# Optimization experiments

Measured on AMD Instinct MI355X. Metric: run time of the kernel, lower is better.

Reference implementation:

```python
import jax, jax.numpy as jnp
import numpy as np

N_NODES = 100000
TYPE_COUNTS = [40000, 40000, 20000]
RAW_DIMS = [512, 256, 128]
D = 64          # node_feature_dim
H = 8           # num_attention_heads
M = 2           # num_metapaths
E = 500000      # edges per metapath
SEM = 128       # semantic_attention_dim
NUM_CLS = 8
T = 40000       # num target nodes
SLOPE = 0.01    # leaky relu slope


def setup_inputs() -> dict:
    key = jax.random.key(0)
    ks = jax.random.split(key, 16)
    inp = {}
    inp['target_nodes'] = jax.random.randint(ks[0], (T,), 0, N_NODES)
    inp['metapath_0'] = jax.random.randint(ks[1], (E, 2), 0, N_NODES)
    inp['metapath_1'] = jax.random.randint(ks[2], (E, 2), 0, N_NODES)
    # contiguous blocks per node type (type t occupies a contiguous index range)
    inp['node_type_mapping'] = jnp.concatenate(
        [jnp.full((c,), t, dtype=jnp.int32) for t, c in enumerate(TYPE_COUNTS)])
    for t, (c, r) in enumerate(zip(TYPE_COUNTS, RAW_DIMS)):
        inp[f'node_feat_{t}'] = jax.random.normal(ks[3 + t], (c, r), dtype=jnp.float32)
        xav = float(np.sqrt(2.0) * np.sqrt(2.0 / (D + r)))
        inp[f'W{t}'] = jax.random.normal(ks[6 + t], (D, r), dtype=jnp.float32) * xav
        inp[f'b{t}'] = jnp.zeros((D,), dtype=jnp.float32)
    inp['node_attention'] = jax.random.normal(ks[9], (M, H, 2 * D), dtype=jnp.float32) * 0.05
    inp['Wsem'] = jax.random.normal(ks[10], (SEM, H * D), dtype=jnp.float32) * 0.05
    inp['bsem'] = jnp.zeros((SEM,), dtype=jnp.float32)
    inp['a_sem'] = jax.random.normal(ks[11], (SEM,), dtype=jnp.float32) * 0.05
    inp['Wcls'] = jax.random.normal(ks[12], (NUM_CLS, H * D), dtype=jnp.float32) * 0.05
    inp['bcls'] = jnp.zeros((NUM_CLS,), dtype=jnp.float32)
    return inp


def _metapath_agg(node_features, mp, attn_vec, target_nodes, n_nodes):
    # mp: [E, 2] (col 0 = neighbor/src, col -1 = current/dst); attn_vec: [H, 2D]
    src = mp[:, 0]
    dst = mp[:, -1]
    h_src = node_features[src]                        # [E, D] gather
    h_dst = node_features[dst]                        # [E, D] gather
    e = jnp.concatenate([h_dst, h_src], axis=-1)      # [E, 2D]
    score = e @ attn_vec.T                            # [E, H]
    score = jnp.where(score > 0, score, SLOPE * score)  # LeakyReLU
    # edge softmax over incoming edges of each destination node (per head)
    m = jax.ops.segment_max(score, dst, num_segments=n_nodes)
    ex = jnp.exp(score - m[dst])
    den = jax.ops.segment_sum(ex, dst, num_segments=n_nodes)
    attn = ex / den[dst]                              # [E, H]
    weighted = h_src[:, None, :] * attn[:, :, None]   # [E, H, D]
    agg = jax.ops.segment_sum(weighted, dst, num_segments=n_nodes)  # [N, H, D]
    return agg[target_nodes]                          # [T, H, D]


def reference(target_nodes, metapath_0, metapath_1, node_type_mapping,
              node_feat_0, node_feat_1, node_feat_2,
              W0, b0, W1, b1, W2, b2,
              node_attention, Wsem, bsem, a_sem, Wcls, bcls):
    n_nodes = node_type_mapping.shape[0]
    # node types are contiguous index blocks, so per-type projection + concat
    # reproduces the original scatter-by-type exactly (dropout rate is 0)
    node_features = jnp.concatenate([
        node_feat_0 @ W0.T + b0,
        node_feat_1 @ W1.T + b1,
        node_feat_2 @ W2.T + b2,
    ], axis=0)                                        # [N, D]
    h_list = [
        _metapath_agg(node_features, metapath_0, node_attention[0], target_nodes, n_nodes),
        _metapath_agg(node_features, metapath_1, node_attention[1], target_nodes, n_nodes),
    ]
    h = jnp.stack(h_list).reshape(M, -1, H * D)       # [M, T, H*D]
    s = jnp.tanh(jnp.einsum('mtd,sd->mts', h, Wsem) + bsem)  # [M, T, SEM]
    scores = jnp.mean(s @ a_sem, axis=1)              # [M] semantic attention
    beta = jax.nn.softmax(scores)                     # [M]
    embeddings = jnp.einsum('m,mtd->td', beta, h)     # [T, H*D]
    cls_logits = embeddings @ Wcls.T + bcls           # [T, NUM_CLS]
    return cls_logits, embeddings
```

## Files before the change

### kernel.cpp

```cpp
#include <hip/hip_runtime.h>
#include <hip/hip_bf16.h>

#define N_NODES 100000
#define EDGES   500000
#define T_TGT   40000
#define NH      8
#define NSEM    128
#define NCLS    8
#define SLOPE   0.01f
#define NCHUNK  25

#define AS1 __attribute__((address_space(1)))
#define AS3 __attribute__((address_space(3)))

typedef __attribute__((ext_vector_type(8))) __bf16 bf16x8;
typedef __attribute__((ext_vector_type(4))) float f32x4;

__global__ __launch_bounds__(256) void proj_gemm(const float* __restrict__ A,
        const float* __restrict__ W, const float* __restrict__ bias,
        float* __restrict__ out, int M, int K) {
    __shared__ float As[32][68];
    __shared__ float Ws[32][68];
    int tid = threadIdx.x;
    int r0 = blockIdx.x * 64;
    int ty = tid >> 4;
    int tx = tid & 15;
    float acc[4][4] = {};
    for (int kk = 0; kk < K; kk += 32) {
        #pragma unroll
        for (int i = 0; i < 2; i++) {
            int lin = tid + i * 256;
            int row = lin >> 3;
            int c4 = (lin & 7) * 4;
            float4 v = make_float4(0.f, 0.f, 0.f, 0.f);
            if (r0 + row < M)
                v = *(const float4*)(A + (size_t)(r0 + row) * K + kk + c4);
            As[c4 + 0][row] = v.x; As[c4 + 1][row] = v.y;
            As[c4 + 2][row] = v.z; As[c4 + 3][row] = v.w;
            float4 w = *(const float4*)(W + (size_t)row * K + kk + c4);
            Ws[c4 + 0][row] = w.x; Ws[c4 + 1][row] = w.y;
            Ws[c4 + 2][row] = w.z; Ws[c4 + 3][row] = w.w;
        }
        __syncthreads();
        #pragma unroll
        for (int k = 0; k < 32; k++) {
            float4 a4 = *(const float4*)&As[k][ty * 4];
            float4 b4 = *(const float4*)&Ws[k][tx * 4];
            float a[4] = {a4.x, a4.y, a4.z, a4.w};
            float b[4] = {b4.x, b4.y, b4.z, b4.w};
            #pragma unroll
            for (int i = 0; i < 4; i++)
                #pragma unroll
                for (int j = 0; j < 4; j++)
                    acc[i][j] = fmaf(a[i], b[j], acc[i][j]);
        }
        __syncthreads();
    }
    float4 b4 = *(const float4*)(bias + tx * 4);
    #pragma unroll
    for (int i = 0; i < 4; i++) {
        int r = r0 + ty * 4 + i;
        if (r < M) {
            float4 o = make_float4(acc[i][0] + b4.x, acc[i][1] + b4.y,
                                   acc[i][2] + b4.z, acc[i][3] + b4.w);
            *(float4*)(out + (size_t)r * 64 + tx * 4) = o;
        }
    }
}

__global__ __launch_bounds__(256) void attn_proj(const float* __restrict__ nf,
        const float* __restrict__ na, float* __restrict__ proj) {
    __shared__ float ft[64][65];
    __shared__ float at[32][65];
    int tid = threadIdx.x;
    int n0 = blockIdx.x * 64;
    #pragma unroll
    for (int i = 0; i < 8; i++) {
        int lin = tid + i * 256;
        int j = lin >> 6, d = lin & 63;
        int m = j >> 4, side = (j >> 3) & 1, h = j & 7;
        at[j][d] = na[m * 1024 + h * 128 + side * 64 + d];
    }
    #pragma unroll
    for (int i = 0; i < 4; i++) {
        int lin = tid + i * 256;
        int row = lin >> 4;
        int c4 = (lin & 15) * 4;
        int gn = n0 + row;
        float4 v = make_float4(0.f, 0.f, 0.f, 0.f);
        if (gn < N_NODES) v = *(const float4*)(nf + (size_t)gn * 64 + c4);
        ft[row][c4 + 0] = v.x; ft[row][c4 + 1] = v.y;
        ft[row][c4 + 2] = v.z; ft[row][c4 + 3] = v.w;
    }
    __syncthreads();
    int node = tid >> 2;
    int jg = tid & 3;
    float acc[8] = {};
    for (int d = 0; d < 64; d++) {
        float f = ft[node][d];
        #pragma unroll
        for (int jj = 0; jj < 8; jj++)
            acc[jj] = fmaf(f, at[jg * 8 + jj][d], acc[jj]);
    }
    int gn = n0 + node;
    if (gn < N_NODES) {
        float4 o0 = make_float4(acc[0], acc[1], acc[2], acc[3]);
        float4 o1 = make_float4(acc[4], acc[5], acc[6], acc[7]);
        *(float4*)(proj + (size_t)gn * 32 + jg * 8) = o0;
        *(float4*)(proj + (size_t)gn * 32 + jg * 8 + 4) = o1;
    }
}

__global__ void hist_targets(const int* __restrict__ tgt, int* __restrict__ tcnt) {
    int i = blockIdx.x * 256 + threadIdx.x;
    if (i < T_TGT) atomicAdd(&tcnt[tgt[i]], 1);
}

__global__ void hist_edges(const int* __restrict__ mp, const int* __restrict__ tcnt,
                           int* __restrict__ ecnt) {
    int e = blockIdx.x * 256 + threadIdx.x;
    if (e < EDGES) {
        int dst = mp[2 * e + 1];
        if (tcnt[dst] > 0) atomicAdd(&ecnt[dst], 1);
    }
}

__global__ __launch_bounds__(1024) void scan_partial(const int* __restrict__ counts,
        int* __restrict__ partials) {
    int a = blockIdx.y, bx = blockIdx.x;
    const int* in = counts + (size_t)a * N_NODES;
    int base = bx * 4096 + threadIdx.x * 4;
    int s = 0;
    #pragma unroll
    for (int i = 0; i < 4; i++) {
        int idx = base + i;
        if (idx < N_NODES) s += in[idx];
    }
    #pragma unroll
    for (int off = 32; off; off >>= 1) s += __shfl_xor(s, off);
    __shared__ int red[16];
    int lane = threadIdx.x & 63, w = threadIdx.x >> 6;
    if (lane == 0) red[w] = s;
    __syncthreads();
    if (threadIdx.x < 16) {
        int x = red[threadIdx.x];
        #pragma unroll
        for (int off = 8; off; off >>= 1) x += __shfl_xor(x, off);
        if (threadIdx.x == 0) partials[a * 32 + bx] = x;
    }
}

__global__ void scan_partials(const int* __restrict__ partials,
        int* __restrict__ choff, int* __restrict__ offs) {
    int w = threadIdx.x >> 6, lane = threadIdx.x & 63;
    if (w < 3 && lane < 32) {
        int v = (lane < NCHUNK) ? partials[w * 32 + lane] : 0;
        int x = v;
        #pragma unroll
        for (int off = 1; off < 32; off <<= 1) {
            int y = __shfl_up(x, off);
            if (lane >= off) x += y;
        }
        if (lane < NCHUNK) choff[w * 32 + lane] = x - v;
        if (lane == NCHUNK - 1) offs[(size_t)w * (N_NODES + 1) + N_NODES] = x;
    }
}

__global__ __launch_bounds__(1024) void scan_final(const int* __restrict__ counts,
        const int* __restrict__ choff, int* __restrict__ offs, int* __restrict__ curs) {
    int a = blockIdx.y, bx = blockIdx.x;
    const int* in = counts + (size_t)a * N_NODES;
    int* out = offs + (size_t)a * (N_NODES + 1);
    int* cur = curs + (size_t)a * N_NODES;
    int tid = threadIdx.x, lane = tid & 63, w = tid >> 6;
    int base = bx * 4096 + tid * 4;
    int v[4], sum4 = 0;
    #pragma unroll
    for (int i = 0; i < 4; i++) {
        int idx = base + i;
        v[i] = (idx < N_NODES) ? in[idx] : 0;
        sum4 += v[i];
    }
    int x = sum4;
    #pragma unroll
    for (int off = 1; off < 64; off <<= 1) {
        int y = __shfl_up(x, off);
        if (lane >= off) x += y;
    }
    __shared__ int wred[16], wexc[16];
    if (lane == 63) wred[w] = x;
    __syncthreads();
    if (tid < 16) {
        int s = wred[tid], xs = s;
        #pragma unroll
        for (int off = 1; off < 16; off <<= 1) {
            int y = __shfl_up(xs, off);
            if (tid >= off) xs += y;
        }
        wexc[tid] = xs - s;
    }
    __syncthreads();
    int off0 = choff[a * 32 + bx] + wexc[w] + (x - sum4);
    int run = 0;
    #pragma unroll
    for (int i = 0; i < 4; i++) {
        int idx = base + i;
        if (idx < N_NODES) { out[idx] = off0 + run; cur[idx] = off0 + run; }
        run += v[i];
    }
}

__global__ void scatter_targets(const int* __restrict__ tgt, int* __restrict__ tcur,
                                int* __restrict__ tlist) {
    int i = blockIdx.x * 256 + threadIdx.x;
    if (i < T_TGT) {
        int n = tgt[i];
        int p = atomicAdd(&tcur[n], 1);
        tlist[p] = i;
    }
}

__global__ __launch_bounds__(256) void scatter_score(const int* __restrict__ mp,
        const int* __restrict__ tcnt, int* __restrict__ ecur,
        int* __restrict__ elist, __bf16* __restrict__ exs,
        const float* __restrict__ proj, int m) {
    int e = blockIdx.x * 256 + threadIdx.x;
    if (e >= EDGES) return;
    int src = mp[2 * e], dst = mp[2 * e + 1];
    if (tcnt[dst] <= 0) return;
    int p = atomicAdd(&ecur[dst], 1);
    elist[p] = src;
    const float* adp = proj + (size_t)dst * 32 + m * 16;
    const float* asp = proj + (size_t)src * 32 + m * 16 + 8;
    float4 ad0 = *(const float4*)(adp), ad1 = *(const float4*)(adp + 4);
    float4 as0 = *(const float4*)(asp), as1 = *(const float4*)(asp + 4);
    float ads[8] = {ad0.x, ad0.y, ad0.z, ad0.w, ad1.x, ad1.y, ad1.z, ad1.w};
    float ass[8] = {as0.x, as0.y, as0.z, as0.w, as1.x, as1.y, as1.z, as1.w};
    bf16x8 exv;
    #pragma unroll
    for (int h = 0; h < 8; h++) {
        float sc = ads[h] + ass[h];
        sc = sc > 0.f ? sc : SLOPE * sc;
        exv[h] = (__bf16)__expf(sc);
    }
    *(bf16x8*)(exs + (size_t)p * 8) = exv;
}

__global__ void build_ulist(const int* __restrict__ tcnt, int* __restrict__ ulist,
                            int* __restrict__ ucount) {
    int n = blockIdx.x * 256 + threadIdx.x;
    if (n < N_NODES && tcnt[n] > 0) {
        int u = atomicAdd(ucount, 1);
        ulist[u] = n;
    }
}

__global__ void cvt_bf16(const float* __restrict__ in, __bf16* __restrict__ out, int n) {
    int i = blockIdx.x * 256 + threadIdx.x;
    if (i < n) out[i] = (__bf16)in[i];
}

__global__ __launch_bounds__(256) void agg_kernel(
        const int* __restrict__ ulist, const int* __restrict__ ctrl_i,
        const int* __restrict__ offs,
        const int* __restrict__ esrc,
        const __bf16* __restrict__ exs,
        const float* __restrict__ nf,
        const int* __restrict__ tlist,
        __bf16* hb0, __bf16* hb1) {
    int m = blockIdx.y;
    int wslot = blockIdx.x * 4 + (threadIdx.x >> 6);
    int lane = threadIdx.x & 63;
    int ucount = ctrl_i[0];
    if (wslot >= ucount) return;
    int node = __builtin_amdgcn_readfirstlane(ulist[wslot]);
    const int* eo = offs + (size_t)m * (N_NODES + 1);
    int e0 = eo[node], e1 = eo[node + 1];
    const int* srcs = esrc + (size_t)m * EDGES;
    const __bf16* exm = exs + (size_t)m * EDGES * 8;
    float acc[8] = {};
    float dacc[8] = {};
    for (int e = e0; e < e1; e++) {
        int s = srcs[e];
        bf16x8 pb = *(const bf16x8*)(exm + (size_t)e * 8);
        float v = nf[(size_t)s * 64 + lane];
        #pragma unroll
        for (int h = 0; h < 8; h++) {
            float pw = (float)pb[h];
            dacc[h] += pw;
            acc[h] = fmaf(pw, v, acc[h]);
        }
    }
    #pragma unroll
    for (int h = 0; h < 8; h++)
        acc[h] *= (dacc[h] > 0.f) ? 1.0f / dacc[h] : 0.f;
    const int* to = offs + (size_t)2 * (N_NODES + 1);
    int t0 = to[node], t1 = to[node + 1];
    __bf16* hb = (m == 0) ? hb0 : hb1;
    for (int ti = t0; ti < t1; ti++) {
        int t = tlist[ti];
        __bf16* dst = hb + (size_t)t * 512;
        #pragma unroll
        for (int h = 0; h < 8; h++) dst[h * 64 + lane] = (__bf16)acc[h];
    }
}

__global__ __launch_bounds__(256) void sem_mfma(
        const __bf16* __restrict__ hb,
        const __bf16* __restrict__ Wb,
        const float* __restrict__ bsem, const float* __restrict__ a_sem,
        float* __restrict__ scores) {
    __shared__ __bf16 As[2][64 * 64];
    __shared__ __bf16 Bs[2][128 * 64];
    int m = blockIdx.y;
    int tid = threadIdx.x;
    int wave = tid >> 6, lane = tid & 63;
    const __bf16* A0 = hb + (size_t)m * T_TGT * 512 + (size_t)blockIdx.x * 64 * 512;

    int srow = lane >> 3;
    int scol = (lane & 7) * 8;

    auto stage = [&](int buf, int k0) {
        #pragma unroll
        for (int j = 0; j < 2; j++) {
            int row = j * 32 + wave * 8 + srow;
            const __bf16* gp = A0 + (size_t)row * 512 + k0 + scol;
            __bf16* lp = &As[buf][(j * 32 + wave * 8) * 64];
            __builtin_amdgcn_global_load_lds((const AS1 void*)gp,
                                             (AS3 void*)lp, 16, 0, 0);
        }
        #pragma unroll
        for (int j = 0; j < 4; j++) {
            int row = j * 32 + wave * 8 + srow;
            const __bf16* gp = Wb + (size_t)row * 512 + k0 + scol;
            __bf16* lp = &Bs[buf][(j * 32 + wave * 8) * 64];
            __builtin_amdgcn_global_load_lds((const AS1 void*)gp,
                                             (AS3 void*)lp, 16, 0, 0);
        }
    };

    int mrow = lane & 15;
    int kq = lane >> 4;
    f32x4 acc[4][2] = {};

    stage(0, 0);
    __syncthreads();
    for (int t = 0; t < 8; t++) {
        int cur = t & 1;
        if (t < 7) stage(cur ^ 1, (t + 1) * 64);
        __builtin_amdgcn_sched_barrier(0);
        const __bf16* Ab = &As[cur][0];
        const __bf16* Bb = &Bs[cur][0];
        #pragma unroll
        for (int kk = 0; kk < 2; kk++) {
            int ko = kk * 32 + kq * 8;
            bf16x8 a[4], b[2];
            #pragma unroll
            for (int r = 0; r < 4; r++)
                a[r] = *(const bf16x8*)(Ab + (r * 16 + mrow) * 64 + ko);
            #pragma unroll
            for (int c = 0; c < 2; c++)
                b[c] = *(const bf16x8*)(Bb + (wave * 32 + c * 16 + mrow) * 64 + ko);
            #pragma unroll
            for (int r = 0; r < 4; r++)
                #pragma unroll
                for (int c = 0; c < 2; c++)
                    acc[r][c] = __builtin_amdgcn_mfma_f32_16x16x32_bf16(a[r], b[c], acc[r][c], 0, 0, 0);
        }
        __syncthreads();
    }

    int n0 = wave * 32;
    float tot = 0.f;
    #pragma unroll
    for (int c = 0; c < 2; c++) {
        int col = n0 + c * 16 + (lane & 15);
        float bs = bsem[col], as = a_sem[col];
        #pragma unroll
        for (int r = 0; r < 4; r++)
            #pragma unroll
            for (int j = 0; j < 4; j++) {
                float x = acc[r][c][j] + bs;
                float th = 1.f - 2.f / (__expf(2.f * x) + 1.f);
                tot += th * as;
            }
    }
    __shared__ float red[256];
    red[threadIdx.x] = tot;
    __syncthreads();
    for (int s = 128; s; s >>= 1) {
        if (threadIdx.x < s) red[threadIdx.x] += red[threadIdx.x + s];
        __syncthreads();
    }
    if (threadIdx.x == 0) atomicAdd(&scores[m], red[0]);
}

__global__ void beta_kernel(const float* __restrict__ scores, float* __restrict__ beta) {
    if (threadIdx.x == 0) {
        float s0 = scores[0] / (float)T_TGT;
        float s1 = scores[1] / (float)T_TGT;
        float mx = fmaxf(s0, s1);
        float e0 = __expf(s0 - mx), e1 = __expf(s1 - mx);
        float inv = 1.f / (e0 + e1);
        beta[0] = e0 * inv;
        beta[1] = e1 * inv;
    }
}

__global__ __launch_bounds__(256) void emb_cls(
        const __bf16* __restrict__ hb0, const __bf16* __restrict__ hb1,
        const float* __restrict__ beta, const float* __restrict__ Wcls,
        const float* __restrict__ bcls, float* out_cls, float* out_emb) {
    __shared__ float Wl[8 * 512];
    int tid = threadIdx.x;
    #pragma unroll
    for (int i = 0; i < 16; i++) Wl[tid + i * 256] = Wcls[tid + i * 256];
    __syncthreads();
    int t = blockIdx.x * 4 + (tid >> 6);
    int lane = tid & 63;
    float b0 = beta[0], b1 = beta[1];
    bf16x8 v0 = *(const bf16x8*)(hb0 + (size_t)t * 512 + lane * 8);
    bf16x8 v1 = *(const bf16x8*)(hb1 + (size_t)t * 512 + lane * 8);
    float e[8];
    #pragma unroll
    for (int j = 0; j < 8; j++) e[j] = b0 * (float)v0[j] + b1 * (float)v1[j];
    float* ep = out_emb + (size_t)t * 512 + lane * 8;
    *(float4*)(ep + 0) = make_float4(e[0], e[1], e[2], e[3]);
    *(float4*)(ep + 4) = make_float4(e[4], e[5], e[6], e[7]);
    float pc[8];
    #pragma unroll
    for (int c = 0; c < 8; c++) {
        float4 w0 = *(const float4*)(Wl + c * 512 + lane * 8);
        float4 w1 = *(const float4*)(Wl + c * 512 + lane * 8 + 4);
        pc[c] = e[0] * w0.x + e[1] * w0.y + e[2] * w0.z + e[3] * w0.w
              + e[4] * w1.x + e[5] * w1.y + e[6] * w1.z + e[7] * w1.w;
    }
    #pragma unroll
    for (int off = 32; off; off >>= 1)
        #pragma unroll
        for (int c = 0; c < 8; c++) pc[c] += __shfl_xor(pc[c], off);
    if (lane == 0) {
        #pragma unroll
        for (int c = 0; c < 8; c++) out_cls[(size_t)t * 8 + c] = pc[c] + bcls[c];
    }
}

extern "C" void kernel_launch(void* const* d_in, const int* in_sizes, int n_in,
                              void* d_out, int out_size, void* d_ws, size_t ws_size,
                              hipStream_t stream) {
    const int* target = (const int*)d_in[0];
    const int* mp0 = (const int*)d_in[1];
    const int* mp1 = (const int*)d_in[2];
    const float* feat0 = (const float*)d_in[4];
    const float* W0 = (const float*)d_in[5];
    const float* b0 = (const float*)d_in[6];
    const float* feat1 = (const float*)d_in[7];
    const float* W1 = (const float*)d_in[8];
    const float* b1 = (const float*)d_in[9];
    const float* feat2 = (const float*)d_in[10];
    const float* W2 = (const float*)d_in[11];
    const float* b2 = (const float*)d_in[12];
    const float* natt = (const float*)d_in[13];
    const float* Wsem = (const float*)d_in[14];
    const float* bsem = (const float*)d_in[15];
    const float* asem = (const float*)d_in[16];
    const float* Wcls = (const float*)d_in[17];
    const float* bcls = (const float*)d_in[18];

    char* ws = (char*)d_ws;
    size_t off = 0;
    auto alloc = [&](size_t bytes) -> void* {
        void* p = ws + off;
        off += (bytes + 31) & ~(size_t)31;
        return p;
    };
    float* nf    = (float*)alloc((size_t)N_NODES * 64 * 4);
    float* proj  = (float*)alloc((size_t)N_NODES * 32 * 4);
    int* counts3 = (int*)alloc((size_t)3 * N_NODES * 4);
    int* offs3   = (int*)alloc((size_t)3 * (N_NODES + 1) * 4);
    int* curs3   = (int*)alloc((size_t)3 * N_NODES * 4);
    int* tlist   = (int*)alloc((size_t)T_TGT * 4);
    int* ulist   = (int*)alloc((size_t)N_NODES * 4);
    int* esrc    = (int*)alloc((size_t)2 * EDGES * 4);
    __bf16* exs  = (__bf16*)alloc((size_t)2 * EDGES * 8 * 2);
    int* partials = (int*)alloc((size_t)3 * 32 * 4);
    int* choff    = (int*)alloc((size_t)3 * 32 * 4);
    int* ctrl    = (int*)alloc(64);
    __bf16* Wsem_b = (__bf16*)alloc((size_t)NSEM * 512 * 2);
    __bf16* hb   = (__bf16*)alloc((size_t)2 * T_TGT * 512 * 2);
    if (off > ws_size) return;

    float* out_cls = (float*)d_out;
    float* out_emb = out_cls + (size_t)T_TGT * NCLS;
    __bf16* hb0 = hb;
    __bf16* hb1 = hb + (size_t)T_TGT * 512;
    float* ctrl_f = (float*)ctrl;
    float* scores = ctrl_f + 1;
    float* beta = ctrl_f + 3;

    hipMemsetAsync(counts3, 0, (size_t)3 * N_NODES * 4, stream);
    hipMemsetAsync(ctrl, 0, 64, stream);

    proj_gemm<<<dim3(625), 256, 0, stream>>>(feat0, W0, b0, nf, 40000, 512);
    proj_gemm<<<dim3(625), 256, 0, stream>>>(feat1, W1, b1, nf + (size_t)40000 * 64, 40000, 256);
    proj_gemm<<<dim3(313), 256, 0, stream>>>(feat2, W2, b2, nf + (size_t)80000 * 64, 20000, 128);
    attn_proj<<<dim3(1563), 256, 0, stream>>>(nf, natt, proj);
    cvt_bf16<<<dim3(256), 256, 0, stream>>>(Wsem, Wsem_b, NSEM * 512);

    hist_targets<<<dim3(157), 256, 0, stream>>>(target, counts3 + 2 * N_NODES);
    hist_edges<<<dim3(1954), 256, 0, stream>>>(mp0, counts3 + 2 * N_NODES, counts3);
    hist_edges<<<dim3(1954), 256, 0, stream>>>(mp1, counts3 + 2 * N_NODES, counts3 + N_NODES);
    scan_partial<<<dim3(NCHUNK, 3), 1024, 0, stream>>>(counts3, partials);
    scan_partials<<<dim3(1), 192, 0, stream>>>(partials, choff, offs3);
    scan_final<<<dim3(NCHUNK, 3), 1024, 0, stream>>>(counts3, choff, offs3, curs3);
    scatter_targets<<<dim3(157), 256, 0, stream>>>(target, curs3 + 2 * N_NODES, tlist);
    scatter_score<<<dim3(1954), 256, 0, stream>>>(mp0, counts3 + 2 * N_NODES, curs3,
                                                  esrc, exs, proj, 0);
    scatter_score<<<dim3(1954), 256, 0, stream>>>(mp1, counts3 + 2 * N_NODES, curs3 + N_NODES,
                                                  esrc + EDGES, exs + (size_t)EDGES * 8, proj, 1);
    build_ulist<<<dim3(391), 256, 0, stream>>>(counts3 + 2 * N_NODES, ulist, ctrl);

    agg_kernel<<<dim3(10000, 2), 256, 0, stream>>>(ulist, ctrl, offs3, esrc, exs,
                                                   nf, tlist, hb0, hb1);
    sem_mfma<<<dim3(625, 2), 256, 0, stream>>>(hb, Wsem_b, bsem, asem, scores);
    beta_kernel<<<dim3(1), 64, 0, stream>>>(scores, beta);
    emb_cls<<<dim3(10000), 256, 0, stream>>>(hb0, hb1, beta, Wcls, bcls, out_cls, out_emb);
}
```

Baseline: 515.5 us.

## Replace fp32 projection GEMMs with merged split-bf16 MFMA kernel

Replaces the three scalar-FMA fp32 projection GEMM launches with one kernel that picks its node type from the block index. Inputs are split into high and low bf16 parts, and three MFMA products approximate fp32 accuracy. LDS tiles are double-buffered so the next global load overlaps the current compute. It trades extra conversion work and LDS traffic for matrix-core throughput and fewer launches, and adds a small precision risk from the bf16x3 split.

```diff
diff --git a/kernel.cpp b/kernel.cpp
--- a/kernel.cpp
+++ b/kernel.cpp
@@ -9,6 +9,7 @@
 #define NCLS    8
 #define SLOPE   0.01f
 #define NCHUNK  25
+#define PPAD    36
 
 #define AS1 __attribute__((address_space(1)))
 #define AS3 __attribute__((address_space(3)))
@@ -16,54 +17,116 @@
 typedef __attribute__((ext_vector_type(8))) __bf16 bf16x8;
 typedef __attribute__((ext_vector_type(4))) float f32x4;
 
-__global__ __launch_bounds__(256) void proj_gemm(const float* __restrict__ A,
-        const float* __restrict__ W, const float* __restrict__ bias,
-        float* __restrict__ out, int M, int K) {
-    __shared__ float As[32][68];
-    __shared__ float Ws[32][68];
+__global__ __launch_bounds__(256) void proj_mfma(
+        const float* __restrict__ A0, const float* __restrict__ W0,
+        const float* __restrict__ b0,
+        const float* __restrict__ A1, const float* __restrict__ W1,
+        const float* __restrict__ b1,
+        const float* __restrict__ A2, const float* __restrict__ W2,
+        const float* __restrict__ b2,
+        float* __restrict__ out) {
+    __shared__ __bf16 Ah[2][128 * PPAD], Al[2][128 * PPAD];
+    __shared__ __bf16 Wh[2][64 * PPAD],  Wl[2][64 * PPAD];
+    int bx = blockIdx.x;
+    const float *A, *W, *bias; int M, K, r0; float* op;
+    if (bx < 313)      { A = A0; W = W0; bias = b0; M = 40000; K = 512;
+                         r0 = bx * 128;         op = out; }
+    else if (bx < 626) { A = A1; W = W1; bias = b1; M = 40000; K = 256;
+                         r0 = (bx - 313) * 128; op = out + (size_t)40000 * 64; }
+    else               { A = A2; W = W2; bias = b2; M = 20000; K = 128;
+                         r0 = (bx - 626) * 128; op = out + (size_t)80000 * 64; }
     int tid = threadIdx.x;
-    int r0 = blockIdx.x * 64;
-    int ty = tid >> 4;
-    int tx = tid & 15;
-    float acc[4][4] = {};
-    for (int kk = 0; kk < K; kk += 32) {
-        #pragma unroll
-        for (int i = 0; i < 2; i++) {
-            int lin = tid + i * 256;
-            int row = lin >> 3;
-            int c4 = (lin & 7) * 4;
-            float4 v = make_float4(0.f, 0.f, 0.f, 0.f);
-            if (r0 + row < M)
-                v = *(const float4*)(A + (size_t)(r0 + row) * K + kk + c4);
-            As[c4 + 0][row] = v.x; As[c4 + 1][row] = v.y;
-            As[c4 + 2][row] = v.z; As[c4 + 3][row] = v.w;
-            float4 w = *(const float4*)(W + (size_t)row * K + kk + c4);
-            Ws[c4 + 0][row] = w.x; Ws[c4 + 1][row] = w.y;
-            Ws[c4 + 2][row] = w.z; Ws[c4 + 3][row] = w.w;
-        }
+    int wave = tid >> 6, lane = tid & 63;
+    int arow = tid >> 1;
+    int acol = (tid & 1) * 16;
+    int wrow = tid & 63;
+    int wcol = wave * 8;
+    const float* Arp = A + (size_t)(r0 + arow) * K + acol;
+    const float* Wrp = W + (size_t)wrow * K + wcol;
+    bool aval = (r0 + arow) < M;
+
+    float4 av0, av1, av2, av3, wv0, wv1;
+    auto gload = [&](int k0) {
+        float4 z = make_float4(0.f, 0.f, 0.f, 0.f);
+        av0 = aval ? *(const float4*)(Arp + k0 + 0)  : z;
+        av1 = aval ? *(const float4*)(Arp + k0 + 4)  : z;
+        av2 = aval ? *(const float4*)(Arp + k0 + 8)  : z;
+        av3 = aval ? *(const float4*)(Arp + k0 + 12) : z;
+        wv0 = *(const float4*)(Wrp + k0 + 0);
+        wv1 = *(const float4*)(Wrp + k0 + 4);
+    };
+    auto cvt_write = [&](int buf) {
+        float xa[16] = {av0.x, av0.y, av0.z, av0.w, av1.x, av1.y, av1.z, av1.w,
+                        av2.x, av2.y, av2.z, av2.w, av3.x, av3.y, av3.z, av3.w};
+        bf16x8 ah2[2], al2[2];
+        #pragma unroll
+        for (int j = 0; j < 16; j++) {
+            __bf16 h = (__bf16)xa[j];
+            ah2[j >> 3][j & 7] = h;
+            al2[j >> 3][j & 7] = (__bf16)(xa[j] - (float)h);
+        }
+        *(bf16x8*)&Ah[buf][arow * PPAD + acol]     = ah2[0];
+        *(bf16x8*)&Ah[buf][arow * PPAD + acol + 8] = ah2[1];
+        *(bf16x8*)&Al[buf][arow * PPAD + acol]     = al2[0];
+        *(bf16x8*)&Al[buf][arow * PPAD + acol + 8] = al2[1];
+        float xw[8] = {wv0.x, wv0.y, wv0.z, wv0.w, wv1.x, wv1.y, wv1.z, wv1.w};
+        bf16x8 wh2, wl2;
+        #pragma unroll
+        for (int j = 0; j < 8; j++) {
+            __bf16 h = (__bf16)xw[j];
+            wh2[j] = h;
+            wl2[j] = (__bf16)(xw[j] - (float)h);
+        }
+        *(bf16x8*)&Wh[buf][wrow * PPAD + wcol] = wh2;
+        *(bf16x8*)&Wl[buf][wrow * PPAD + wcol] = wl2;
+    };
+
+    int mrow = lane & 15, koff = (lane >> 4) * 8;
+    f32x4 acc[2][4] = {};
+    int nsteps = K >> 5;
+
+    gload(0);
+    cvt_write(0);
+    __syncthreads();
+    for (int t = 0; t < nsteps; t++) {
+        int cur = t & 1;
+        if (t + 1 < nsteps) gload((t + 1) * 32);
+        __builtin_amdgcn_sched_barrier(0);
+        bf16x8 afh[2], afl[2], bfh[4], bfl[4];
+        #pragma unroll
+        for (int mi = 0; mi < 2; mi++) {
+            int r = wave * 32 + mi * 16 + mrow;
+            afh[mi] = *(const bf16x8*)&Ah[cur][r * PPAD + koff];
+            afl[mi] = *(const bf16x8*)&Al[cur][r * PPAD + koff];
+        }
+        #pragma unroll
+        for (int ni = 0; ni < 4; ni++) {
+            int r = ni * 16 + mrow;
+            bfh[ni] = *(const bf16x8*)&Wh[cur][r * PPAD + koff];
+            bfl[ni] = *(const bf16x8*)&Wl[cur][r * PPAD + koff];
+        }
+        #pragma unroll
+        for (int mi = 0; mi < 2; mi++)
+            #pragma unroll
+            for (int ni = 0; ni < 4; ni++) {
+                acc[mi][ni] = __builtin_amdgcn_mfma_f32_16x16x32_bf16(afh[mi], bfh[ni], acc[mi][ni], 0, 0, 0);
+                acc[mi][ni] = __builtin_amdgcn_mfma_f32_16x16x32_bf16(afh[mi], bfl[ni], acc[mi][ni], 0, 0, 0);
+                acc[mi][ni] = __builtin_amdgcn_mfma_f32_16x16x32_bf16(afl[mi], bfh[ni], acc[mi][ni], 0, 0, 0);
+            }
+        if (t + 1 < nsteps) cvt_write(cur ^ 1);
         __syncthreads();
-        #pragma unroll
-        for (int k = 0; k < 32; k++) {
-            float4 a4 = *(const float4*)&As[k][ty * 4];
-            float4 b4 = *(const float4*)&Ws[k][tx * 4];
-            float a[4] = {a4.x, a4.y, a4.z, a4.w};
-            float b[4] = {b4.x, b4.y, b4.z, b4.w};
+    }
+    #pragma unroll
+    for (int ni = 0; ni < 4; ni++) {
+        int col = ni * 16 + mrow;
+        float bv = bias[col];
+        #pragma unroll
+        for (int mi = 0; mi < 2; mi++) {
+            int row = r0 + wave * 32 + mi * 16 + (lane >> 4) * 4;
             #pragma unroll
-            for (int i = 0; i < 4; i++)
-                #pragma unroll
-                for (int j = 0; j < 4; j++)
-                    acc[i][j] = fmaf(a[i], b[j], acc[i][j]);
-        }
-        __syncthreads();
-    }
-    float4 b4 = *(const float4*)(bias + tx * 4);
-    #pragma unroll
-    for (int i = 0; i < 4; i++) {
-        int r = r0 + ty * 4 + i;
-        if (r < M) {
-            float4 o = make_float4(acc[i][0] + b4.x, acc[i][1] + b4.y,
-                                   acc[i][2] + b4.z, acc[i][3] + b4.w);
-            *(float4*)(out + (size_t)r * 64 + tx * 4) = o;
+            for (int j = 0; j < 4; j++)
+                if (row + j < M)
+                    op[(size_t)(row + j) * 64 + col] = acc[mi][ni][j] + bv;
         }
     }
 }
@@ -501,9 +564,8 @@
     hipMemsetAsync(counts3, 0, (size_t)3 * N_NODES * 4, stream);
     hipMemsetAsync(ctrl, 0, 64, stream);
 
-    proj_gemm<<<dim3(625), 256, 0, stream>>>(feat0, W0, b0, nf, 40000, 512);
-    proj_gemm<<<dim3(625), 256, 0, stream>>>(feat1, W1, b1, nf + (size_t)40000 * 64, 40000, 256);
-    proj_gemm<<<dim3(313), 256, 0, stream>>>(feat2, W2, b2, nf + (size_t)80000 * 64, 20000, 128);
+    proj_mfma<<<dim3(783), 256, 0, stream>>>(feat0, W0, b0, feat1, W1, b1,
+                                             feat2, W2, b2, nf);
     attn_proj<<<dim3(1563), 256, 0, stream>>>(nf, natt, proj);
     cvt_bf16<<<dim3(256), 256, 0, stream>>>(Wsem, Wsem_b, NSEM * 512);
 
```

Measured after the change: 524.3 us. About the same (+1.7%).
